# Optimization experiments

Measured on AMD Instinct MI355X. Metric: run time of the kernel, lower is better.

The kernel has to match this reference:

```python
import jax, jax.numpy as jnp
import numpy as np
from jax import lax

B, T, D, H, L = 64, 1024, 256, 1024, 2


def setup_inputs() -> dict:
    key = jax.random.key(0)
    ks = jax.random.split(key, 9)
    s = 0.03  # small init so tanh/sigmoid stay in sane range
    return {
        "x": jax.random.normal(ks[0], (B, T, D), dtype=jnp.float32),
        "W_ih0": jax.random.normal(ks[1], (4 * H, D), dtype=jnp.float32) * s,
        "W_hh0": jax.random.normal(ks[2], (4 * H, H), dtype=jnp.float32) * s,
        "b_ih0": jax.random.normal(ks[3], (4 * H,), dtype=jnp.float32) * s,
        "b_hh0": jax.random.normal(ks[4], (4 * H,), dtype=jnp.float32) * s,
        "W_ih1": jax.random.normal(ks[5], (4 * H, H), dtype=jnp.float32) * s,
        "W_hh1": jax.random.normal(ks[6], (4 * H, H), dtype=jnp.float32) * s,
        "b_ih1": jax.random.normal(ks[7], (4 * H,), dtype=jnp.float32) * s,
        "b_hh1": jax.random.normal(ks[8], (4 * H,), dtype=jnp.float32) * s,
    }


def _lstm_layer(x, W_ih, W_hh, b_ih, b_hh):
    """Single LSTM layer over full sequence. x: [B,T,Din]. Returns (ys [B,T,H], h [B,H], c [B,H])."""
    b, t = x.shape[0], x.shape[1]
    h_dim = W_hh.shape[1]
    # Precompute input projections for all timesteps in one GEMM.
    xg = jnp.einsum('bti,gi->btg', x, W_ih) + b_ih + b_hh  # [B,T,4H]

    def step(carry, xg_t):
        h, c = carry
        g = xg_t + h @ W_hh.T  # [B,4H]
        i, f, gg, o = jnp.split(g, 4, axis=-1)  # PyTorch gate order i,f,g,o
        i = jax.nn.sigmoid(i)
        f = jax.nn.sigmoid(f)
        gg = jnp.tanh(gg)
        o = jax.nn.sigmoid(o)
        c = f * c + i * gg
        h = o * jnp.tanh(c)
        return (h, c), h

    h0 = jnp.zeros((b, h_dim), x.dtype)
    (h, c), ys = lax.scan(step, (h0, h0), jnp.swapaxes(xg, 0, 1))
    return jnp.swapaxes(ys, 0, 1), h, c


def reference(x, W_ih0, W_hh0, b_ih0, b_hh0, W_ih1, W_hh1, b_ih1, b_hh1):
    # Dropout layers are identity in eval mode; nn.LSTM inter-layer dropout
    # is also inactive in eval, so the math is a plain stacked LSTM whose
    # final (h, c) per layer is returned, matching the torch forward().
    y0, h0_, c0_ = _lstm_layer(x, W_ih0, W_hh0, b_ih0, b_hh0)
    _, h1_, c1_ = _lstm_layer(y0, W_ih1, W_hh1, b_ih1, b_hh1)
    h = jnp.stack([h0_, h1_], axis=0)  # [L,B,H]
    c = jnp.stack([c0_, c1_], axis=0)  # [L,B,H]
    return (h, c)
```

## Files before the change

kernel.cpp:

```cpp
#include <hip/hip_runtime.h>

#define NWG     256
#define TPB     256
#define NL0     128
#define T_STEPS 1024
#define HD      1024
#define DIN     256
#define K0      1280
#define K1      2048
#define K0P     1288
#define K1P     2056
#define SMEM_BYTES (32*K1P*2)

#define HSLAB_BYTES 131072ull
#define HSLAB_U64   16384
#define HIST_DEPTH  1025
#define HIST_BYTES  (HIST_DEPTH*HSLAB_BYTES)
#define X8_BYTES    33554432ull
#define FLAGS_BYTES 32768ull
#define NGEN        16

typedef float  f32x4  __attribute__((ext_vector_type(4)));
typedef __bf16 bf16x8 __attribute__((ext_vector_type(8)));
typedef unsigned long long u64;

__device__ __forceinline__ unsigned short f2bf(float f){
  union { float f; unsigned u; } a; a.f = f;
  unsigned u = a.u;
  u += 0x7fffu + ((u >> 16) & 1u);
  return (unsigned short)(u >> 16);
}
__device__ __forceinline__ float sigmf(float x){ return 1.0f/(1.0f + __expf(-x)); }
__device__ __forceinline__ float tanhf_fast(float x){ return 2.0f*sigmf(2.0f*x) - 1.0f; }

__device__ __forceinline__ u64 ld64c(const u64* p){
  return __hip_atomic_load(p, __ATOMIC_RELAXED, __HIP_MEMORY_SCOPE_AGENT);
}
__device__ __forceinline__ void st16c(unsigned short* p, unsigned short v){
  __hip_atomic_store(p, v, __ATOMIC_RELAXED, __HIP_MEMORY_SCOPE_AGENT);
}
__device__ __forceinline__ unsigned ldflag(const unsigned* p){
  return __hip_atomic_load(p, __ATOMIC_RELAXED, __HIP_MEMORY_SCOPE_AGENT);
}
__device__ __forceinline__ void stflag(unsigned* p, unsigned v){
  __hip_atomic_store(p, v, __ATOMIC_RELAXED, __HIP_MEMORY_SCOPE_AGENT);
}

__device__ __forceinline__ void gridbar(unsigned* flags, unsigned* gen,
                                        unsigned ep, int wg, int tid){
  asm volatile("s_waitcnt vmcnt(0)" ::: "memory");
  __syncthreads();
  if (wg == 0){
    if (tid > 0){
      while (ldflag(&flags[tid*16]) < ep) __builtin_amdgcn_s_sleep(4);
    }
    __syncthreads();
    if (tid < NGEN) stflag(&gen[tid*16], ep);
    __syncthreads();
  } else {
    if (tid == 0){
      stflag(&flags[wg*16], ep);
      while (ldflag(&gen[(wg & (NGEN-1))*16]) < ep) __builtin_amdgcn_s_sleep(4);
    }
    __syncthreads();
  }
}

__global__ void xpose_kernel(const float* __restrict__ x, unsigned short* __restrict__ X8){
  int idx   = blockIdx.x*256 + threadIdx.x;
  int t     = idx >> 11;
  int rem   = idx & 2047;
  int plane = rem >> 6;
  int b     = rem & 63;
  const float* src = x + ((size_t)b << 18) + (t << 8) + (plane << 3);
  unsigned short tmp[8];
  #pragma unroll
  for (int j = 0; j < 8; ++j) tmp[j] = f2bf(src[j]);
  int4 v; __builtin_memcpy(&v, tmp, 16);
  ((int4*)X8)[idx] = v;
}

template<bool H0C, bool H1C>
__global__ void __launch_bounds__(TPB, 1)
lstm_mega(const float* __restrict__ Wih0, const float* __restrict__ Whh0,
          const float* __restrict__ bih0, const float* __restrict__ bhh0,
          const float* __restrict__ Wih1, const float* __restrict__ Whh1,
          const float* __restrict__ bih1, const float* __restrict__ bhh1,
          const unsigned short* __restrict__ X8,
          unsigned* flags, unsigned* gen,
          u64* H0, u64* H1, int d0, int d1,
          float* __restrict__ out)
{
  extern __shared__ unsigned short Ws[];
  const int tid   = threadIdx.x;
  const int wg    = blockIdx.x;
  const int layer = (wg >= NL0);
  const int wgl   = layer ? wg - NL0 : wg;
  const int KD    = layer ? K1  : K0;
  const int dlen  = layer ? HD  : DIN;
  const int KP    = layer ? K1P : K0P;
  const int4* X4  = (const int4*)X8;

  {
    const float* Wih = layer ? Wih1 : Wih0;
    const float* Whh = layer ? Whh1 : Whh0;
    for (int m = 0; m < 32; ++m){
      int gr = (m & 3)*HD + wgl*8 + (m >> 2);
      const float* ar = Wih + (size_t)gr*dlen;
      const float* br = Whh + (size_t)gr*HD;
      unsigned short* row = Ws + m*KP;
      for (int k = tid; k < KD; k += TPB)
        row[k] = f2bf(k < dlen ? ar[k] : br[k - dlen]);
    }
  }
  __syncthreads();

  const int lane  = tid & 63;
  const int wv    = tid >> 6;
  const int q     = lane >> 4;
  const int nn    = lane & 15;
  const int batch = wv*16 + nn;

  float bias[2][4];
  {
    const float* bi = layer ? bih1 : bih0;
    const float* bh = layer ? bhh1 : bhh0;
    #pragma unroll
    for (int rt = 0; rt < 2; ++rt){
      int colr = wgl*8 + rt*4 + q;
      #pragma unroll
      for (int r = 0; r < 4; ++r)
        bias[rt][r] = bi[r*HD + colr] + bh[r*HD + colr];
    }
  }

  float cst[2] = {0.f, 0.f};
  float hv[2]  = {0.f, 0.f};

  auto do_step = [&](int t){
    f32x4 a00 = {0,0,0,0}, a01 = {0,0,0,0}, a10 = {0,0,0,0}, a11 = {0,0,0,0};

    auto MM = [&](int kb, bf16x8 b){
      bf16x8 a0, a1;
      __builtin_memcpy(&a0, &Ws[nn*KP + kb*32 + q*8], 16);
      __builtin_memcpy(&a1, &Ws[(16+nn)*KP + kb*32 + q*8], 16);
      if (kb & 1){ a01 = __builtin_amdgcn_mfma_f32_16x16x32_bf16(a0,b,a01,0,0,0);
                   a11 = __builtin_amdgcn_mfma_f32_16x16x32_bf16(a1,b,a11,0,0,0); }
      else       { a00 = __builtin_amdgcn_mfma_f32_16x16x32_bf16(a0,b,a00,0,0,0);
                   a10 = __builtin_amdgcn_mfma_f32_16x16x32_bf16(a1,b,a10,0,0,0); }
    };

    if (!layer){
      const int4* xb = X4 + (size_t)t*2048;
      const u64* hb  = H0 + (size_t)(t % d0)*HSLAB_U64;

      int4 xr[8];
      #pragma unroll
      for (int kb = 0; kb < 8; ++kb)
        xr[kb] = xb[(kb*4 + q)*64 + batch];

      u64 B[3][16];
      auto LD = [&](int c){
        u64* d = B[c % 3];
        #pragma unroll
        for (int i = 0; i < 8; ++i){
          const u64* p = hb + (((c*8 + i)*4 + q)*64 + batch)*2;
          d[2*i]   = H0C ? ld64c(p)     : p[0];
          d[2*i+1] = H0C ? ld64c(p + 1) : p[1];
        }
      };
      LD(0); LD(1);
      #pragma unroll
      for (int kb = 0; kb < 8; ++kb){
        bf16x8 b; __builtin_memcpy(&b, &xr[kb], 16);
        MM(kb, b);
      }
      LD(2);
      #pragma unroll
      for (int c = 0; c < 4; ++c){
        u64* d = B[c % 3];
        #pragma unroll
        for (int i = 0; i < 8; ++i){
          u64 pair[2] = {d[2*i], d[2*i+1]};
          bf16x8 b; __builtin_memcpy(&b, pair, 16);
          MM(8 + c*8 + i, b);
        }
        if (c + 3 < 4) LD(c + 3);
      }
    } else {
      const u64* yb = H0 + (size_t)((t+1) % d0)*HSLAB_U64;
      const u64* hb = H1 + (size_t)(t % d1)*HSLAB_U64;

      u64 B[3][16];
      auto LD = [&](int c){
        const u64* src = (c < 4) ? yb : hb;
        int p0 = (c & 3)*8;
        u64* d = B[c % 3];
        #pragma unroll
        for (int i = 0; i < 8; ++i){
          const u64* p = src + (((p0 + i)*4 + q)*64 + batch)*2;
          if (c < 4){ d[2*i] = H0C ? ld64c(p) : p[0];
                      d[2*i+1] = H0C ? ld64c(p + 1) : p[1]; }
          else      { d[2*i] = H1C ? ld64c(p) : p[0];
                      d[2*i+1] = H1C ? ld64c(p + 1) : p[1]; }
        }
      };
      LD(0); LD(1); LD(2);
      #pragma unroll
      for (int c = 0; c < 8; ++c){
        u64* d = B[c % 3];
        #pragma unroll
        for (int i = 0; i < 8; ++i){
          u64 pair[2] = {d[2*i], d[2*i+1]};
          bf16x8 b; __builtin_memcpy(&b, pair, 16);
          MM(c*8 + i, b);
        }
        if (c + 3 < 8) LD(c + 3);
      }
    }

    f32x4 s0 = a00 + a01, s1 = a10 + a11;
    u64* Hw = layer ? H1 : H0;
    int  wd = layer ? d1 : d0;
    unsigned short* wbase = (unsigned short*)(Hw + (size_t)((t+1) % wd)*HSLAB_U64);
    #pragma unroll
    for (int rt = 0; rt < 2; ++rt){
      f32x4 s = rt ? s1 : s0;
      float ii = sigmf(s[0] + bias[rt][0]);
      float ff = sigmf(s[1] + bias[rt][1]);
      float gg = tanhf_fast(s[2] + bias[rt][2]);
      float oo = sigmf(s[3] + bias[rt][3]);
      cst[rt] = ff*cst[rt] + ii*gg;
      hv[rt]  = oo*tanhf_fast(cst[rt]);
      st16c(wbase + (wgl*64 + batch)*8 + (rt*4 + q), f2bf(hv[rt]));
    }
  };

  if (!layer){
    for (int s = 0; s < T_STEPS; ++s){
      do_step(s);
      gridbar(flags, gen, (unsigned)(s+1), wg, tid);
    }
  } else {
    for (int s = 0; s < T_STEPS; ++s){
      if (s > 0) do_step(s-1);
      gridbar(flags, gen, (unsigned)(s+1), wg, tid);
    }
    do_step(T_STEPS-1);
  }

  {
    int col0 = wgl*8 + q;
    int base = layer ? 65536 : 0;
    out[base          + batch*HD + col0    ] = hv[0];
    out[base          + batch*HD + col0 + 4] = hv[1];
    out[base + 131072 + batch*HD + col0    ] = cst[0];
    out[base + 131072 + batch*HD + col0 + 4] = cst[1];
  }
}

extern "C" void kernel_launch(void* const* d_in, const int* in_sizes, int n_in,
                              void* d_out, int out_size, void* d_ws, size_t ws_size,
                              hipStream_t stream)
{
  const float* x    = (const float*)d_in[0];
  const float* Wih0 = (const float*)d_in[1];
  const float* Whh0 = (const float*)d_in[2];
  const float* bih0 = (const float*)d_in[3];
  const float* bhh0 = (const float*)d_in[4];
  const float* Wih1 = (const float*)d_in[5];
  const float* Whh1 = (const float*)d_in[6];
  const float* bih1 = (const float*)d_in[7];
  const float* bhh1 = (const float*)d_in[8];
  float* out = (float*)d_out;

  char* ws = (char*)d_ws;
  unsigned* flags = (unsigned*)ws;
  unsigned* gen   = (unsigned*)(ws + 16384);

  const size_t need2 = FLAGS_BYTES + 2*HIST_BYTES + X8_BYTES;
  const size_t need1 = FLAGS_BYTES + HIST_BYTES + 2*HSLAB_BYTES + X8_BYTES;

  u64 *H0p, *H1p; unsigned short* X8p; int d0, d1, tier;
  if (ws_size >= need2){
    tier = 2; d0 = HIST_DEPTH; d1 = HIST_DEPTH;
    H0p = (u64*)(ws + FLAGS_BYTES);
    H1p = (u64*)(ws + FLAGS_BYTES + HIST_BYTES);
    X8p = (unsigned short*)(ws + FLAGS_BYTES + 2*HIST_BYTES);
  } else if (ws_size >= need1){
    tier = 1; d0 = HIST_DEPTH; d1 = 2;
    H0p = (u64*)(ws + FLAGS_BYTES);
    H1p = (u64*)(ws + FLAGS_BYTES + HIST_BYTES);
    X8p = (unsigned short*)(ws + FLAGS_BYTES + HIST_BYTES + 2*HSLAB_BYTES);
  } else {
    tier = 0; d0 = 2; d1 = 2;
    H0p = (u64*)(ws + FLAGS_BYTES);
    H1p = (u64*)(ws + FLAGS_BYTES + 2*HSLAB_BYTES);
    X8p = (unsigned short*)(ws + FLAGS_BYTES + 4*HSLAB_BYTES);
  }

  hipMemsetAsync(flags, 0, FLAGS_BYTES, stream);
  hipMemsetAsync(H0p, 0, HSLAB_BYTES, stream);
  hipMemsetAsync(H1p, 0, HSLAB_BYTES, stream);
  xpose_kernel<<<8192, 256, 0, stream>>>(x, X8p);

  void* fn = (tier == 2) ? (void*)&lstm_mega<false,false>
           : (tier == 1) ? (void*)&lstm_mega<false,true>
                         : (void*)&lstm_mega<true,true>;
  hipFuncSetAttribute(fn, hipFuncAttributeMaxDynamicSharedMemorySize, SMEM_BYTES);

  const unsigned short* X8c = X8p;
  void* args[] = {(void*)&Wih0,(void*)&Whh0,(void*)&bih0,(void*)&bhh0,
                  (void*)&Wih1,(void*)&Whh1,(void*)&bih1,(void*)&bhh1,
                  (void*)&X8c,(void*)&flags,(void*)&gen,
                  (void*)&H0p,(void*)&H1p,(void*)&d0,(void*)&d1,(void*)&out};
  hipError_t err = hipLaunchCooperativeKernel(fn, dim3(NWG), dim3(TPB),
                                              args, SMEM_BYTES, stream);
  if (err != hipSuccess){
    if (tier == 2)
      lstm_mega<false,false><<<dim3(NWG), dim3(TPB), SMEM_BYTES, stream>>>(
        Wih0,Whh0,bih0,bhh0,Wih1,Whh1,bih1,bhh1,X8c,flags,gen,H0p,H1p,d0,d1,out);
    else if (tier == 1)
      lstm_mega<false,true><<<dim3(NWG), dim3(TPB), SMEM_BYTES, stream>>>(
        Wih0,Whh0,bih0,bhh0,Wih1,Whh1,bih1,bhh1,X8c,flags,gen,H0p,H1p,d0,d1,out);
    else
      lstm_mega<true,true><<<dim3(NWG), dim3(TPB), SMEM_BYTES, stream>>>(
        Wih0,Whh0,bih0,bhh0,Wih1,Whh1,bih1,bhh1,X8c,flags,gen,H0p,H1p,d0,d1,out);
  }
}
```

Baseline: 6.613 ms.

## Split grid barrier into per-layer barriers with layer-1 waiting on layer-0 generation

Replaces the single all-workgroup barrier per timestep with separate barriers for the layer-0 and layer-1 workgroup sets, each with its own generation counter. Layer 1 first loads its own recurrent h, then spins only on layer 0's generation before loading layer 0's output, so the two layers can run decoupled with layer 1 lagging. H loads are issued as full 16-byte loads up front when history buffers allow plain loads, and spin sleep intervals are shortened. Relies on the history-depth buffers so layer 0 can run ahead without overwriting data layer 1 still needs; the small-workspace tier keeps the old lockstep scheme.

Measured after the change: 10.19 ms. 54.1% more time.

```diff
diff --git a/kernel.cpp b/kernel.cpp
--- a/kernel.cpp
+++ b/kernel.cpp
@@ -46,13 +46,29 @@
   __hip_atomic_store(p, v, __ATOMIC_RELAXED, __HIP_MEMORY_SCOPE_AGENT);
 }
 
-__device__ __forceinline__ void gridbar(unsigned* flags, unsigned* gen,
-                                        unsigned ep, int wg, int tid){
+template<bool PLAIN>
+__device__ __forceinline__ int4 ldh(const u64* p){
+  int4 v;
+  if (PLAIN){
+    v = *(const int4*)p;
+  } else {
+    u64 lo = ld64c(p), hi = ld64c(p + 1);
+    __builtin_memcpy(&v, &lo, 8);
+    __builtin_memcpy(((char*)&v) + 8, &hi, 8);
+  }
+  return v;
+}
+__device__ __forceinline__ bf16x8 b8(const int4& v){
+  bf16x8 b; __builtin_memcpy(&b, &v, 16); return b;
+}
+
+__device__ __forceinline__ void gridbar_all(unsigned* flags, unsigned* gen,
+                                            unsigned ep, int wg, int tid){
   asm volatile("s_waitcnt vmcnt(0)" ::: "memory");
   __syncthreads();
   if (wg == 0){
     if (tid > 0){
-      while (ldflag(&flags[tid*16]) < ep) __builtin_amdgcn_s_sleep(4);
+      while (ldflag(&flags[tid*16]) < ep) __builtin_amdgcn_s_sleep(2);
     }
     __syncthreads();
     if (tid < NGEN) stflag(&gen[tid*16], ep);
@@ -60,7 +76,27 @@
   } else {
     if (tid == 0){
       stflag(&flags[wg*16], ep);
-      while (ldflag(&gen[(wg & (NGEN-1))*16]) < ep) __builtin_amdgcn_s_sleep(4);
+      while (ldflag(&gen[(wg & (NGEN-1))*16]) < ep) __builtin_amdgcn_s_sleep(2);
+    }
+    __syncthreads();
+  }
+}
+
+__device__ __forceinline__ void layerbar(unsigned* flags, unsigned* gen,
+                                         unsigned ep, int wg, int tid, int base){
+  asm volatile("s_waitcnt vmcnt(0)" ::: "memory");
+  __syncthreads();
+  if (wg == base){
+    if (tid > 0 && tid < NL0){
+      while (ldflag(&flags[(base + tid)*16]) < ep) __builtin_amdgcn_s_sleep(2);
+    }
+    __syncthreads();
+    if (tid < NGEN) stflag(&gen[tid*16], ep);
+    __syncthreads();
+  } else {
+    if (tid == 0){
+      stflag(&flags[wg*16], ep);
+      while (ldflag(&gen[(wg & (NGEN-1))*16]) < ep) __builtin_amdgcn_s_sleep(2);
     }
     __syncthreads();
   }
@@ -80,14 +116,14 @@
   ((int4*)X8)[idx] = v;
 }
 
-template<bool H0C, bool H1C>
+template<int TIER>
 __global__ void __launch_bounds__(TPB, 1)
 lstm_mega(const float* __restrict__ Wih0, const float* __restrict__ Whh0,
           const float* __restrict__ bih0, const float* __restrict__ bhh0,
           const float* __restrict__ Wih1, const float* __restrict__ Whh1,
           const float* __restrict__ bih1, const float* __restrict__ bhh1,
           const unsigned short* __restrict__ X8,
-          unsigned* flags, unsigned* gen,
+          unsigned* flags, unsigned* gen0, unsigned* gen1,
           u64* H0, u64* H1, int d0, int d1,
           float* __restrict__ out)
 {
@@ -137,91 +173,7 @@
   float cst[2] = {0.f, 0.f};
   float hv[2]  = {0.f, 0.f};
 
-  auto do_step = [&](int t){
-    f32x4 a00 = {0,0,0,0}, a01 = {0,0,0,0}, a10 = {0,0,0,0}, a11 = {0,0,0,0};
-
-    auto MM = [&](int kb, bf16x8 b){
-      bf16x8 a0, a1;
-      __builtin_memcpy(&a0, &Ws[nn*KP + kb*32 + q*8], 16);
-      __builtin_memcpy(&a1, &Ws[(16+nn)*KP + kb*32 + q*8], 16);
-      if (kb & 1){ a01 = __builtin_amdgcn_mfma_f32_16x16x32_bf16(a0,b,a01,0,0,0);
-                   a11 = __builtin_amdgcn_mfma_f32_16x16x32_bf16(a1,b,a11,0,0,0); }
-      else       { a00 = __builtin_amdgcn_mfma_f32_16x16x32_bf16(a0,b,a00,0,0,0);
-                   a10 = __builtin_amdgcn_mfma_f32_16x16x32_bf16(a1,b,a10,0,0,0); }
-    };
-
-    if (!layer){
-      const int4* xb = X4 + (size_t)t*2048;
-      const u64* hb  = H0 + (size_t)(t % d0)*HSLAB_U64;
-
-      int4 xr[8];
-      #pragma unroll
-      for (int kb = 0; kb < 8; ++kb)
-        xr[kb] = xb[(kb*4 + q)*64 + batch];
-
-      u64 B[3][16];
-      auto LD = [&](int c){
-        u64* d = B[c % 3];
-        #pragma unroll
-        for (int i = 0; i < 8; ++i){
-          const u64* p = hb + (((c*8 + i)*4 + q)*64 + batch)*2;
-          d[2*i]   = H0C ? ld64c(p)     : p[0];
-          d[2*i+1] = H0C ? ld64c(p + 1) : p[1];
-        }
-      };
-      LD(0); LD(1);
-      #pragma unroll
-      for (int kb = 0; kb < 8; ++kb){
-        bf16x8 b; __builtin_memcpy(&b, &xr[kb], 16);
-        MM(kb, b);
-      }
-      LD(2);
-      #pragma unroll
-      for (int c = 0; c < 4; ++c){
-        u64* d = B[c % 3];
-        #pragma unroll
-        for (int i = 0; i < 8; ++i){
-          u64 pair[2] = {d[2*i], d[2*i+1]};
-          bf16x8 b; __builtin_memcpy(&b, pair, 16);
-          MM(8 + c*8 + i, b);
-        }
-        if (c + 3 < 4) LD(c + 3);
-      }
-    } else {
-      const u64* yb = H0 + (size_t)((t+1) % d0)*HSLAB_U64;
-      const u64* hb = H1 + (size_t)(t % d1)*HSLAB_U64;
-
-      u64 B[3][16];
-      auto LD = [&](int c){
-        const u64* src = (c < 4) ? yb : hb;
-        int p0 = (c & 3)*8;
-        u64* d = B[c % 3];
-        #pragma unroll
-        for (int i = 0; i < 8; ++i){
-          const u64* p = src + (((p0 + i)*4 + q)*64 + batch)*2;
-          if (c < 4){ d[2*i] = H0C ? ld64c(p) : p[0];
-                      d[2*i+1] = H0C ? ld64c(p + 1) : p[1]; }
-          else      { d[2*i] = H1C ? ld64c(p) : p[0];
-                      d[2*i+1] = H1C ? ld64c(p + 1) : p[1]; }
-        }
-      };
-      LD(0); LD(1); LD(2);
-      #pragma unroll
-      for (int c = 0; c < 8; ++c){
-        u64* d = B[c % 3];
-        #pragma unroll
-        for (int i = 0; i < 8; ++i){
-          u64 pair[2] = {d[2*i], d[2*i+1]};
-          bf16x8 b; __builtin_memcpy(&b, pair, 16);
-          MM(c*8 + i, b);
-        }
-        if (c + 3 < 8) LD(c + 3);
-      }
-    }
-
-    f32x4 s0 = a00 + a01, s1 = a10 + a11;
-    u64* Hw = layer ? H1 : H0;
-    int  wd = layer ? d1 : d0;
+  auto epi = [&](int t, f32x4 s0, f32x4 s1, u64* Hw, int wd){
     unsigned short* wbase = (unsigned short*)(Hw + (size_t)((t+1) % wd)*HSLAB_U64);
     #pragma unroll
     for (int rt = 0; rt < 2; ++rt){
@@ -237,16 +189,110 @@
   };
 
   if (!layer){
-    for (int s = 0; s < T_STEPS; ++s){
-      do_step(s);
-      gridbar(flags, gen, (unsigned)(s+1), wg, tid);
-    }
-  } else {
-    for (int s = 0; s < T_STEPS; ++s){
-      if (s > 0) do_step(s-1);
-      gridbar(flags, gen, (unsigned)(s+1), wg, tid);
-    }
-    do_step(T_STEPS-1);
+    for (int t = 0; t < T_STEPS; ++t){
+      const int4* xb = X4 + (size_t)t*2048;
+      const u64*  hb = H0 + (size_t)(t % d0)*HSLAB_U64;
+
+      int4 xr[8];
+      #pragma unroll
+      for (int kb = 0; kb < 8; ++kb)
+        xr[kb] = xb[(kb*4 + q)*64 + batch];
+
+      int4 Bh[4][8];
+      #pragma unroll
+      for (int c = 0; c < 4; ++c)
+        #pragma unroll
+        for (int i = 0; i < 8; ++i)
+          Bh[c][i] = ldh<(TIER >= 1)>(hb + (((c*8 + i)*4 + q)*64 + batch)*2);
+
+      f32x4 a00={0,0,0,0}, a01={0,0,0,0}, a10={0,0,0,0}, a11={0,0,0,0};
+      auto MM = [&](int kb, bf16x8 b){
+        bf16x8 w0, w1;
+        __builtin_memcpy(&w0, &Ws[nn*K0P + kb*32 + q*8], 16);
+        __builtin_memcpy(&w1, &Ws[(16+nn)*K0P + kb*32 + q*8], 16);
+        if (kb & 1){ a01 = __builtin_amdgcn_mfma_f32_16x16x32_bf16(w0,b,a01,0,0,0);
+                     a11 = __builtin_amdgcn_mfma_f32_16x16x32_bf16(w1,b,a11,0,0,0); }
+        else       { a00 = __builtin_amdgcn_mfma_f32_16x16x32_bf16(w0,b,a00,0,0,0);
+                     a10 = __builtin_amdgcn_mfma_f32_16x16x32_bf16(w1,b,a10,0,0,0); }
+      };
+      #pragma unroll
+      for (int kb = 0; kb < 8; ++kb) MM(kb, b8(xr[kb]));
+      #pragma unroll
+      for (int c = 0; c < 4; ++c)
+        #pragma unroll
+        for (int i = 0; i < 8; ++i) MM(8 + c*8 + i, b8(Bh[c][i]));
+
+      epi(t, a00 + a01, a10 + a11, H0, d0);
+      if (TIER > 0) layerbar(flags, gen0, (unsigned)(t+1), wg, tid, 0);
+      else          gridbar_all(flags, gen0, (unsigned)(t+1), wg, tid);
+    }
+  } else {
+    auto stepL1 = [&](int t, bool dowait){
+      const u64* hb = H1 + (size_t)(t % d1)*HSLAB_U64;
+      const u64* yb = H0 + (size_t)((t+1) % d0)*HSLAB_U64;
+
+      int4 Bh[4][8];
+      auto LDH = [&](int c){
+        #pragma unroll
+        for (int i = 0; i < 8; ++i)
+          Bh[c][i] = ldh<(TIER == 2)>(hb + (((c*8 + i)*4 + q)*64 + batch)*2);
+      };
+      LDH(0); LDH(1); LDH(2); LDH(3);
+
+      if (dowait){
+        while (ldflag(&gen0[(wg & (NGEN-1))*16]) < (unsigned)(t+1))
+          __builtin_amdgcn_s_sleep(1);
+      }
+
+      int4 By[4][8];
+      auto LDY = [&](int c){
+        #pragma unroll
+        for (int i = 0; i < 8; ++i)
+          By[c][i] = ldh<(TIER >= 1)>(yb + (((c*8 + i)*4 + q)*64 + batch)*2);
+      };
+
+      f32x4 a00={0,0,0,0}, a01={0,0,0,0}, a10={0,0,0,0}, a11={0,0,0,0};
+      auto MM = [&](int kb, bf16x8 b){
+        bf16x8 w0, w1;
+        __builtin_memcpy(&w0, &Ws[nn*K1P + kb*32 + q*8], 16);
+        __builtin_memcpy(&w1, &Ws[(16+nn)*K1P + kb*32 + q*8], 16);
+        if (kb & 1){ a01 = __builtin_amdgcn_mfma_f32_16x16x32_bf16(w0,b,a01,0,0,0);
+                     a11 = __builtin_amdgcn_mfma_f32_16x16x32_bf16(w1,b,a11,0,0,0); }
+        else       { a00 = __builtin_amdgcn_mfma_f32_16x16x32_bf16(w0,b,a00,0,0,0);
+                     a10 = __builtin_amdgcn_mfma_f32_16x16x32_bf16(w1,b,a10,0,0,0); }
+      };
+
+      LDY(0); LDY(1);
+      #pragma unroll
+      for (int i = 0; i < 8; ++i) MM(32 + i,      b8(Bh[0][i]));
+      LDY(2);
+      #pragma unroll
+      for (int i = 0; i < 8; ++i) MM(32 + 8 + i,  b8(Bh[1][i]));
+      LDY(3);
+      #pragma unroll
+      for (int c = 2; c < 4; ++c)
+        #pragma unroll
+        for (int i = 0; i < 8; ++i) MM(32 + c*8 + i, b8(Bh[c][i]));
+      #pragma unroll
+      for (int c = 0; c < 4; ++c)
+        #pragma unroll
+        for (int i = 0; i < 8; ++i) MM(c*8 + i, b8(By[c][i]));
+
+      epi(t, a00 + a01, a10 + a11, H1, d1);
+    };
+
+    if (TIER > 0){
+      for (int t = 0; t < T_STEPS; ++t){
+        stepL1(t, true);
+        layerbar(flags, gen1, (unsigned)(t+1), wg, tid, NL0);
+      }
+    } else {
+      for (int s = 0; s < T_STEPS; ++s){
+        if (s > 0) stepL1(s-1, false);
+        gridbar_all(flags, gen0, (unsigned)(s+1), wg, tid);
+      }
+      stepL1(T_STEPS-1, false);
+    }
   }
 
   {
@@ -276,7 +322,8 @@
 
   char* ws = (char*)d_ws;
   unsigned* flags = (unsigned*)ws;
-  unsigned* gen   = (unsigned*)(ws + 16384);
+  unsigned* gen0  = (unsigned*)(ws + 16384);
+  unsigned* gen1  = (unsigned*)(ws + 20480);
 
   const size_t need2 = FLAGS_BYTES + 2*HIST_BYTES + X8_BYTES;
   const size_t need1 = FLAGS_BYTES + HIST_BYTES + 2*HSLAB_BYTES + X8_BYTES;
@@ -304,27 +351,27 @@
   hipMemsetAsync(H1p, 0, HSLAB_BYTES, stream);
   xpose_kernel<<<8192, 256, 0, stream>>>(x, X8p);
 
-  void* fn = (tier == 2) ? (void*)&lstm_mega<false,false>
-           : (tier == 1) ? (void*)&lstm_mega<false,true>
-                         : (void*)&lstm_mega<true,true>;
+  void* fn = (tier == 2) ? (void*)&lstm_mega<2>
+           : (tier == 1) ? (void*)&lstm_mega<1>
+                         : (void*)&lstm_mega<0>;
   hipFuncSetAttribute(fn, hipFuncAttributeMaxDynamicSharedMemorySize, SMEM_BYTES);
 
   const unsigned short* X8c = X8p;
   void* args[] = {(void*)&Wih0,(void*)&Whh0,(void*)&bih0,(void*)&bhh0,
                   (void*)&Wih1,(void*)&Whh1,(void*)&bih1,(void*)&bhh1,
-                  (void*)&X8c,(void*)&flags,(void*)&gen,
+                  (void*)&X8c,(void*)&flags,(void*)&gen0,(void*)&gen1,
                   (void*)&H0p,(void*)&H1p,(void*)&d0,(void*)&d1,(void*)&out};
   hipError_t err = hipLaunchCooperativeKernel(fn, dim3(NWG), dim3(TPB),
                                               args, SMEM_BYTES, stream);
   if (err != hipSuccess){
     if (tier == 2)
-      lstm_mega<false,false><<<dim3(NWG), dim3(TPB), SMEM_BYTES, stream>>>(
-        Wih0,Whh0,bih0,bhh0,Wih1,Whh1,bih1,bhh1,X8c,flags,gen,H0p,H1p,d0,d1,out);
+      lstm_mega<2><<<dim3(NWG), dim3(TPB), SMEM_BYTES, stream>>>(
+        Wih0,Whh0,bih0,bhh0,Wih1,Whh1,bih1,bhh1,X8c,flags,gen0,gen1,H0p,H1p,d0,d1,out);
     else if (tier == 1)
-      lstm_mega<false,true><<<dim3(NWG), dim3(TPB), SMEM_BYTES, stream>>>(
-        Wih0,Whh0,bih0,bhh0,Wih1,Whh1,bih1,bhh1,X8c,flags,gen,H0p,H1p,d0,d1,out);
+      lstm_mega<1><<<dim3(NWG), dim3(TPB), SMEM_BYTES, stream>>>(
+        Wih0,Whh0,bih0,bhh0,Wih1,Whh1,bih1,bhh1,X8c,flags,gen0,gen1,H0p,H1p,d0,d1,out);
     else
-      lstm_mega<true,true><<<dim3(NWG), dim3(TPB), SMEM_BYTES, stream>>>(
-        Wih0,Whh0,bih0,bhh0,Wih1,Whh1,bih1,bhh1,X8c,flags,gen,H0p,H1p,d0,d1,out);
-  }
-}
+      lstm_mega<0><<<dim3(NWG), dim3(TPB), SMEM_BYTES, stream>>>(
+        Wih0,Whh0,bih0,bhh0,Wih1,Whh1,bih1,bhh1,X8c,flags,gen0,gen1,H0p,H1p,d0,d1,out);
+  }
+}
```
